# Optimization experiments

Measured on AMD Instinct MI355X. Metric: run time of the kernel, lower is better.

The kernel has to match this reference:

```python
import jax, jax.numpy as jnp
import numpy as np

DIM = 1024
SEQ_LEN = 4096
K = 256
HEADS = 16
DIM_HEAD = DIM // HEADS  # 64
BATCH = 4


def setup_inputs() -> dict:
    key = jax.random.key(0)
    ks = jax.random.split(key, 8)
    x = jax.random.normal(ks[0], (BATCH, SEQ_LEN, DIM), dtype=jnp.float32)
    # nn.Linear weights are [out, in]; y = x @ W.T
    std_lin = 1.0 / np.sqrt(DIM)
    Wq = jax.random.uniform(ks[1], (HEADS * DIM_HEAD, DIM), minval=-std_lin, maxval=std_lin, dtype=jnp.float32)
    Wk = jax.random.uniform(ks[2], (HEADS * DIM_HEAD, DIM), minval=-std_lin, maxval=std_lin, dtype=jnp.float32)
    Wv = jax.random.uniform(ks[3], (HEADS * DIM_HEAD, DIM), minval=-std_lin, maxval=std_lin, dtype=jnp.float32)
    # proj_k/proj_v init_: uniform(-1/sqrt(k), 1/sqrt(k)) on [seq_len, k]
    std_p = 1.0 / np.sqrt(K)
    proj_k = jax.random.uniform(ks[4], (SEQ_LEN, K), minval=-std_p, maxval=std_p, dtype=jnp.float32)
    proj_v = jax.random.uniform(ks[5], (SEQ_LEN, K), minval=-std_p, maxval=std_p, dtype=jnp.float32)
    std_o = 1.0 / np.sqrt(HEADS * DIM_HEAD)
    Wo = jax.random.uniform(ks[6], (DIM, HEADS * DIM_HEAD), minval=-std_o, maxval=std_o, dtype=jnp.float32)
    bo = jax.random.uniform(ks[7], (DIM,), minval=-std_o, maxval=std_o, dtype=jnp.float32)
    return {"x": x, "Wq": Wq, "Wk": Wk, "Wv": Wv, "proj_k": proj_k, "proj_v": proj_v, "Wo": Wo, "bo": bo}


def reference(x, Wq, Wk, Wv, proj_k, proj_v, Wo, bo):
    b, n, d = x.shape
    h, dh, k = HEADS, DIM_HEAD, K
    # q/k/v projections
    q = jnp.einsum('bnd,ed->bne', x, Wq)            # [b, n, h*dh]
    keys = jnp.einsum('bnd,ed->bne', x, Wk)         # [b, n, h*dh]
    vals = jnp.einsum('bnd,ed->bne', x, Wv)         # [b, n, h*dh]
    # low-rank projection along sequence: [b, n, e] x [n, k] -> [b, k, e]
    keys = jnp.einsum('bne,nk->bke', keys, proj_k[:n])
    vals = jnp.einsum('bne,nk->bke', vals, proj_v[:n])
    # split heads
    q = q.reshape(b, n, h, dh).transpose(0, 2, 1, 3)        # [b, h, n, dh]
    keys = keys.reshape(b, k, h, dh).transpose(0, 2, 1, 3)  # [b, h, k, dh]
    vals = vals.reshape(b, k, h, dh).transpose(0, 2, 1, 3)  # [b, h, k, dh]
    dots = jnp.einsum('bhnd,bhkd->bhnk', q, keys) * (dh ** -0.5)
    attn = jax.nn.softmax(dots, axis=-1)
    out = jnp.einsum('bhnk,bhkd->bhnd', attn, vals)
    out = out.transpose(0, 2, 1, 3).reshape(b, n, h * dh)
    return jnp.einsum('bne,oe->bno', out, Wo) + bo
```

## Files before the change

### kernel.cpp

```cpp
#include <hip/hip_runtime.h>
#include <hip/hip_bf16.h>
#include <stdint.h>

typedef unsigned short u16;
typedef __attribute__((ext_vector_type(8))) short bf16x8;
typedef __attribute__((ext_vector_type(4))) float f32x4;

#define DEV __device__ __forceinline__

DEV u16 f2bf(float f) {
  union { float f; unsigned u; } v; v.f = f;
  unsigned r = (v.u + 0x7fffu + ((v.u >> 16) & 1u)) >> 16;
  return (u16)r;
}

DEV float bf2f(u16 h) {
  union { unsigned u; float f; } v; v.u = ((unsigned)h) << 16;
  return v.f;
}

DEV unsigned pk2(float lo, float hi) {
  union { __hip_bfloat162 h; unsigned u; } c;
  c.h = __float22bfloat162_rn(make_float2(lo, hi));
  return c.u;
}

DEV f32x4 mfma16(bf16x8 a, bf16x8 b, f32x4 c) {
  return __builtin_amdgcn_mfma_f32_16x16x32_bf16(a, b, c, 0, 0, 0);
}

DEV void gload_lds16(const u16* g, u16* l) {
  __builtin_amdgcn_global_load_lds((const __attribute__((address_space(1))) void*)g,
                                   (__attribute__((address_space(3))) void*)l, 16, 0, 0);
}

#define QSCALE 0.18033688011112042f

__global__ void cvt_xpose_kernel(const float* __restrict__ src, u16* __restrict__ dst_rm,
                                 u16* __restrict__ dst_tp, int R, int C,
                                 long zS, long zRM, long zTP) {
  __shared__ u16 tile[64][72];
  src += (size_t)blockIdx.z * zS;
  dst_tp += (size_t)blockIdx.z * zTP;
  int r0 = blockIdx.y * 64, c0 = blockIdx.x * 64;
  int tr = threadIdx.x >> 2, tc = (threadIdx.x & 3) * 16;
  const float* s = src + (size_t)(r0 + tr) * C + c0 + tc;
  u16 loc[16];
#pragma unroll
  for (int q = 0; q < 4; ++q) {
    float4 v = ((const float4*)s)[q];
    loc[q * 4 + 0] = f2bf(v.x); loc[q * 4 + 1] = f2bf(v.y);
    loc[q * 4 + 2] = f2bf(v.z); loc[q * 4 + 3] = f2bf(v.w);
  }
#pragma unroll
  for (int i = 0; i < 16; ++i) tile[tr][tc + i] = loc[i];
  if (dst_rm) {
    u16* d = dst_rm + (size_t)blockIdx.z * zRM + (size_t)(r0 + tr) * C + c0 + tc;
    *(bf16x8*)d = *(const bf16x8*)&loc[0];
    *(bf16x8*)(d + 8) = *(const bf16x8*)&loc[8];
  }
  __syncthreads();
  u16 tmp[16];
#pragma unroll
  for (int i = 0; i < 16; ++i) tmp[i] = tile[tc + i][tr];
  u16* d = dst_tp + (size_t)(c0 + tr) * R + r0 + tc;
  *(bf16x8*)d = *(const bf16x8*)&tmp[0];
  *(bf16x8*)(d + 8) = *(const bf16x8*)&tmp[8];
}

__global__ void cvt_misc_kernel(const float* __restrict__ s0, const float* __restrict__ s1,
                                const float* __restrict__ s2, const float* __restrict__ s3,
                                u16* __restrict__ d0, u16* __restrict__ d1,
                                u16* __restrict__ d2, u16* __restrict__ d3,
                                const float* __restrict__ pk, const float* __restrict__ pv,
                                u16* __restrict__ projT) {
  __shared__ u16 tile[64][72];
  const int y = blockIdx.y;
  if (y < 4) {
    const float* s; u16* d;
    switch (y) {
      case 0: s = s0; d = d0; break;
      case 1: s = s1; d = d1; break;
      case 2: s = s2; d = d2; break;
      default: s = s3; d = d3; break;
    }
    int i = blockIdx.x * 256 + threadIdx.x;
    float4 v = ((const float4*)s)[i];
    ushort4 o; o.x = f2bf(v.x); o.y = f2bf(v.y); o.z = f2bf(v.z); o.w = f2bf(v.w);
    ((ushort4*)d)[i] = o;
    return;
  }
  if (blockIdx.x >= 256) return;
  const float* src = (y == 4) ? pk : pv;
  u16* dst = projT + (size_t)(y - 4) * 1048576;
  int r0 = (blockIdx.x >> 2) * 64, c0 = (blockIdx.x & 3) * 64;
  int tr = threadIdx.x >> 2, tc = (threadIdx.x & 3) * 16;
  const float* s = src + (size_t)(r0 + tr) * 256 + c0 + tc;
  u16 loc[16];
#pragma unroll
  for (int q = 0; q < 4; ++q) {
    float4 v = ((const float4*)s)[q];
    loc[q * 4 + 0] = f2bf(v.x); loc[q * 4 + 1] = f2bf(v.y);
    loc[q * 4 + 2] = f2bf(v.z); loc[q * 4 + 3] = f2bf(v.w);
  }
#pragma unroll
  for (int i = 0; i < 16; ++i) tile[tr][tc + i] = loc[i];
  __syncthreads();
  u16 tmp[16];
#pragma unroll
  for (int i = 0; i < 16; ++i) tmp[i] = tile[tc + i][tr];
  u16* d = dst + (size_t)(c0 + tr) * 4096 + r0 + tc;
  *(bf16x8*)d = *(const bf16x8*)&tmp[0];
  *(bf16x8*)(d + 8) = *(const bf16x8*)&tmp[8];
}

__global__ void reduce4_kernel(const u16* __restrict__ part, u16* __restrict__ out) {
  int i = blockIdx.x * 256 + threadIdx.x;
  bf16x8 a = ((const bf16x8*)part)[i];
  bf16x8 b = ((const bf16x8*)part)[i + 262144];
  bf16x8 c = ((const bf16x8*)part)[i + 524288];
  bf16x8 d = ((const bf16x8*)part)[i + 786432];
  u16 o[8];
#pragma unroll
  for (int j = 0; j < 8; ++j)
    o[j] = f2bf(bf2f((u16)a[j]) + bf2f((u16)b[j]) + bf2f((u16)c[j]) + bf2f((u16)d[j]));
  ((bf16x8*)out)[i] = *(const bf16x8*)&o[0];
}

template<int OMODE>
__global__ __launch_bounds__(256, 4)
void gemm_bt_kernel(const u16* __restrict__ A, const u16* __restrict__ Bt,
                    const u16* __restrict__ Bt2, void* __restrict__ Cout,
                    u16* __restrict__ CoutT, const float* __restrict__ bias, float cscale,
                    int ldA, int ldB, int ldC, int Klen,
                    long zA, long zB, long zC, int bMod, long kChunkA, long kChunkB) {
  __shared__ __align__(16) u16 smA[2][128 * 32];
  __shared__ __align__(16) u16 smB[2][128 * 32];
  const int t = threadIdx.x;
  const int lane = t & 63, wave = t >> 6;
  const int wm = wave & 1, wn = wave >> 1;
  const int g = lane >> 4, r = lane & 15;
  const int id = blockIdx.y * gridDim.x + blockIdx.x;
  const int cpx = (gridDim.x * gridDim.y) >> 3;
  const int s = (id & 7) * cpx + (id >> 3);
  const int bx = s % gridDim.x, by = s / gridDim.x;
  const int z = blockIdx.z;
  const int b = z % bMod, kc = z / bMod;
  const u16* Ab = A + (size_t)b * zA + (size_t)kc * kChunkA;
  const u16* Bbase = (Bt2 && (b & 1)) ? Bt2 : Bt;
  const u16* Bb = Bbase + (size_t)b * zB + (size_t)kc * kChunkB;
  const int m0 = by * 128, n0 = bx * 128;
  const int srow = t >> 2;
  const int lslot = ((t & 3) + 4 - ((srow >> 1) & 3)) & 3;

  f32x4 acc[4][4];
#pragma unroll
  for (int m = 0; m < 4; ++m)
#pragma unroll
    for (int n = 0; n < 4; ++n) acc[m][n] = f32x4{0.f, 0.f, 0.f, 0.f};

  auto STAGE = [&](int buf, int k0) {
#pragma unroll
    for (int p = 0; p < 2; ++p) {
      int row = p * 64 + srow;
      gload_lds16(Ab + (size_t)(m0 + row) * ldA + k0 + lslot * 8, &smA[buf][p * 2048 + wave * 512]);
      gload_lds16(Bb + (size_t)(n0 + row) * ldB + k0 + lslot * 8, &smB[buf][p * 2048 + wave * 512]);
    }
  };

  const int nt = Klen >> 5;
  STAGE(0, 0);
  __syncthreads();
  int cur = 0;
  for (int it = 0; it < nt; ++it) {
    if (it + 1 < nt) STAGE(cur ^ 1, (it + 1) << 5);
    bf16x8 af[4], bfr[4];
#pragma unroll
    for (int m = 0; m < 4; ++m) {
      int row = wm * 64 + m * 16 + r;
      int ps = (g + (row >> 1)) & 3;
      af[m] = *(const bf16x8*)&smA[cur][row * 32 + ps * 8];
    }
#pragma unroll
    for (int n = 0; n < 4; ++n) {
      int row = wn * 64 + n * 16 + r;
      int ps = (g + (row >> 1)) & 3;
      bfr[n] = *(const bf16x8*)&smB[cur][row * 32 + ps * 8];
    }
#pragma unroll
    for (int m = 0; m < 4; ++m)
#pragma unroll
      for (int n = 0; n < 4; ++n)
        acc[m][n] = mfma16(af[m], bfr[n], acc[m][n]);
    __syncthreads();
    cur ^= 1;
  }

  if constexpr (OMODE == 4) {
    u16* myT = (u16*)&smA[0][0] + wave * 4096;
    u16* Cg = (u16*)Cout + (size_t)z * zC + (size_t)(m0 + wm * 64) * ldC + n0 + wn * 64;
#pragma unroll
    for (int m = 0; m < 4; ++m)
#pragma unroll
      for (int n = 0; n < 4; ++n)
#pragma unroll
        for (int rr = 0; rr < 4; ++rr) {
          int rl = m * 16 + 4 * g + rr;
          int cl = n * 16 + r;
          myT[rl * 64 + (((cl >> 3) ^ (rl & 7)) << 3) + (cl & 7)] = f2bf(acc[m][n][rr]);
        }
#pragma unroll
    for (int i = 0; i < 8; ++i) {
      int idx = i * 64 + lane;
      int row = idx >> 3, c8 = idx & 7;
      bf16x8 v = *(const bf16x8*)&myT[row * 64 + ((c8 ^ (row & 7)) << 3)];
      *(bf16x8*)&Cg[(size_t)row * ldC + c8 * 8] = v;
    }
  } else {
    if ((z & 1) == 0) {
      u16* C = (u16*)Cout + (size_t)(z >> 1) * zC;
#pragma unroll
      for (int n = 0; n < 4; ++n) {
        int col = n0 + wn * 64 + n * 16 + r;
#pragma unroll
        for (int m = 0; m < 4; ++m) {
          int rowb = m0 + wm * 64 + m * 16 + 4 * g;
#pragma unroll
          for (int rr = 0; rr < 4; ++rr)
            C[(size_t)(rowb + rr) * ldC + col] = f2bf(acc[m][n][rr]);
        }
      }
    } else {
      u16* C = CoutT + (size_t)(z >> 1) * zC;
#pragma unroll
      for (int n = 0; n < 4; ++n) {
        int col = n0 + wn * 64 + n * 16 + r;
#pragma unroll
        for (int m = 0; m < 4; ++m) {
          int rowb = m0 + wm * 64 + m * 16 + 4 * g;
          ushort4 o;
          o.x = f2bf(acc[m][n][0]); o.y = f2bf(acc[m][n][1]);
          o.z = f2bf(acc[m][n][2]); o.w = f2bf(acc[m][n][3]);
          *(ushort4*)&C[(size_t)col * 256 + rowb] = o;
        }
      }
    }
  }
}

template<int OMODE>
__global__ __launch_bounds__(256, 2)
void qgemm64_kernel(const u16* __restrict__ A, const u16* __restrict__ Bt,
                    void* __restrict__ Cout, const float* __restrict__ bias,
                    float cscale, int ldA, int ldB, int ldC, int Klen) {
  __shared__ __align__(16) u16 lds[32768];
  const int t = threadIdx.x;
  const int lane = t & 63, wave = t >> 6;
  const int g = lane >> 4, r = lane & 15;
  const int wm = wave >> 1, wn = wave & 1;
  const int id = blockIdx.y * gridDim.x + blockIdx.x;
  const int cpx = (gridDim.x * gridDim.y) >> 3;
  const int s = (id & 7) * cpx + (id >> 3);
  const int bx = s & 7, by = s >> 3;
  const int m0 = by * 128, n0 = bx * 128;

  auto STAGE = [&](int buf, int k0) {
#pragma unroll
    for (int j = 0; j < 4; ++j) {
      int u = j * 256 + t;
      int row = u >> 3, psl = u & 7;
      int sl = (psl + 8 - (row & 7)) & 7;
      gload_lds16(A + (size_t)(m0 + row) * ldA + k0 + sl * 8,
                  lds + buf * 16384 + u * 8);
    }
#pragma unroll
    for (int j = 0; j < 4; ++j) {
      int u = j * 256 + t;
      int row = u >> 3, psl = u & 7;
      int sl = (psl + 8 - (row & 7)) & 7;
      gload_lds16(Bt + (size_t)(n0 + row) * ldB + k0 + sl * 8,
                  lds + buf * 16384 + 8192 + u * 8);
    }
  };

  f32x4 acc[4][4];
#pragma unroll
  for (int m = 0; m < 4; ++m)
#pragma unroll
    for (int n = 0; n < 4; ++n) acc[m][n] = f32x4{0.f, 0.f, 0.f, 0.f};

  const int nt = Klen >> 6;
  STAGE(0, 0);
  asm volatile("s_waitcnt vmcnt(0)" ::: "memory");
  __builtin_amdgcn_s_barrier();

  int cur = 0;
  for (int it = 0; it < nt; ++it) {
    if (it + 1 < nt) STAGE(cur ^ 1, (it + 1) << 6);
    const u16* Ab = lds + cur * 16384;
    const u16* Bb = Ab + 8192;
    bf16x8 af[4][2], bfr[4][2];
#pragma unroll
    for (int m = 0; m < 4; ++m) {
      int row = wm * 64 + m * 16 + r;
      af[m][0] = *(const bf16x8*)&Ab[row * 64 + (((g + row) & 7) << 3)];
      af[m][1] = *(const bf16x8*)&Ab[row * 64 + (((4 + g + row) & 7) << 3)];
    }
#pragma unroll
    for (int n = 0; n < 4; ++n) {
      int row = wn * 64 + n * 16 + r;
      bfr[n][0] = *(const bf16x8*)&Bb[row * 64 + (((g + row) & 7) << 3)];
      bfr[n][1] = *(const bf16x8*)&Bb[row * 64 + (((4 + g + row) & 7) << 3)];
    }
#pragma unroll
    for (int m = 0; m < 4; ++m)
#pragma unroll
      for (int n = 0; n < 4; ++n) {
        acc[m][n] = mfma16(af[m][0], bfr[n][0], acc[m][n]);
        acc[m][n] = mfma16(af[m][1], bfr[n][1], acc[m][n]);
      }
    if (it + 1 < nt) {
      asm volatile("s_waitcnt vmcnt(0)" ::: "memory");
      __builtin_amdgcn_s_barrier();
    }
    cur ^= 1;
  }
  __builtin_amdgcn_s_barrier();

  if constexpr (OMODE == 0) {
    u16* myT = lds + wave * 4096;
    u16* Cg = (u16*)Cout + (size_t)(m0 + wm * 64) * ldC + n0 + wn * 64;
#pragma unroll
    for (int m = 0; m < 4; ++m)
#pragma unroll
      for (int n = 0; n < 4; ++n)
#pragma unroll
        for (int rr = 0; rr < 4; ++rr) {
          int rl = m * 16 + 4 * g + rr;
          int cl = n * 16 + r;
          myT[rl * 64 + (((cl >> 3) ^ (rl & 7)) << 3) + (cl & 7)] = f2bf(acc[m][n][rr] * cscale);
        }
#pragma unroll
    for (int i = 0; i < 8; ++i) {
      int idx = i * 64 + lane;
      int row = idx >> 3, c8 = idx & 7;
      bf16x8 v = *(const bf16x8*)&myT[row * 64 + ((c8 ^ (row & 7)) << 3)];
      *(bf16x8*)&Cg[(size_t)row * ldC + c8 * 8] = v;
    }
  } else {
    float* myF = (float*)lds + wave * 2048;
    float bvn[4];
#pragma unroll
    for (int n = 0; n < 4; ++n) bvn[n] = bias[n0 + wn * 64 + n * 16 + r];
    float* Cg = (float*)Cout + (size_t)(m0 + wm * 64) * ldC + n0 + wn * 64;
#pragma unroll
    for (int np = 0; np < 2; ++np) {
#pragma unroll
      for (int n2 = 0; n2 < 2; ++n2)
#pragma unroll
        for (int m = 0; m < 4; ++m)
#pragma unroll
          for (int rr = 0; rr < 4; ++rr) {
            int rl = m * 16 + 4 * g + rr;
            int cl = n2 * 16 + r;
            myF[rl * 32 + ((((cl >> 2) ^ (rl & 7)) & 7) << 2) + (cl & 3)] =
                acc[m][np * 2 + n2][rr] + bvn[np * 2 + n2];
          }
#pragma unroll
      for (int i = 0; i < 8; ++i) {
        int idx = i * 64 + lane;
        int row = idx >> 3, c = idx & 7;
        float4 v = *(const float4*)&myF[row * 32 + (((c ^ (row & 7)) & 7) << 2)];
        *(float4*)&Cg[(size_t)row * ldC + np * 32 + c * 4] = v;
      }
    }
  }
}

__global__ __launch_bounds__(256, 3)
void attn_kernel(const u16* __restrict__ Q, const u16* __restrict__ Kl,
                 const u16* __restrict__ VT, u16* __restrict__ Out) {
  __shared__ __align__(16) u16 sm[24576];
  const int t = threadIdx.x, lane = t & 63, w = t >> 6;
  const int g = lane >> 4, r = lane & 15;
  const int id = (blockIdx.y << 6) | blockIdx.x;
  const int s = (id & 7) * (gridDim.y << 3) + (id >> 3);
  const int b = blockIdx.z, h = s >> 6, n0 = (s & 63) * 64;
  const u16* Kb = Kl + (size_t)b * 262144 + h * 64;
  const u16* Vb = VT + (size_t)b * 262144 + (size_t)(h * 64) * 256;
  u16* vbase = sm + 16384;

  auto stage_slice = [&](int sl64, int buf) {
#pragma unroll
    for (int i = 0; i < 2; ++i) {
      int u = i * 256 + t;
      int d = u >> 3, ps = u & 7;
      gload_lds16(Vb + (size_t)d * 256 + sl64 * 64 + (ps ^ (d & 7)) * 8,
                  vbase + buf * 4096 + i * 2048 + t * 8);
    }
  };

#pragma unroll
  for (int p = 0; p < 8; ++p) {
    int row = p * 32 + (t >> 3);
    int ls = ((t & 7) + 8 - (row & 7)) & 7;
    gload_lds16(Kb + (size_t)row * 1024 + ls * 8, sm + p * 2048 + w * 512);
  }
  stage_slice(0, 0);
  stage_slice(1, 1);
  const int qrow = n0 + w * 16 + r;
  const u16* Qp = Q + ((size_t)(b * 4096 + qrow)) * 1024 + h * 64 + g * 8;
  bf16x8 aq0 = *(const bf16x8*)Qp;
  bf16x8 aq1 = *(const bf16x8*)(Qp + 32);
  asm volatile("s_waitcnt vmcnt(4)" ::: "memory");
  __builtin_amdgcn_s_barrier();

  f32x4 dotv[16];
  __builtin_amdgcn_s_setprio(1);
#pragma unroll
  for (int kf = 0; kf < 16; ++kf) {
    int row = kf * 16 + r;
    bf16x8 kb0 = *(const bf16x8*)&sm[row * 64 + ((g + row) & 7) * 8];
    bf16x8 kb1 = *(const bf16x8*)&sm[row * 64 + ((4 + g + row) & 7) * 8];
    f32x4 d = f32x4{0.f, 0.f, 0.f, 0.f};
    d = mfma16(kb0, aq0, d);
    d = mfma16(kb1, aq1, d);
    dotv[kf] = d;
  }
  __builtin_amdgcn_s_setprio(0);
  asm volatile("s_waitcnt vmcnt(2)" ::: "memory");
  __builtin_amdgcn_s_barrier();

  float mx = -3.4e38f;
#pragma unroll
  for (int kf = 0; kf < 16; ++kf)
    mx = fmaxf(mx, fmaxf(fmaxf(dotv[kf][0], dotv[kf][1]), fmaxf(dotv[kf][2], dotv[kf][3])));
  mx = fmaxf(mx, __shfl_xor(mx, 16, 64));
  mx = fmaxf(mx, __shfl_xor(mx, 32, 64));
  float ssum = 0.f;
#pragma unroll
  for (int kf = 0; kf < 16; ++kf)
#pragma unroll
    for (int j = 0; j < 4; ++j) {
      float p = __builtin_amdgcn_exp2f(dotv[kf][j] - mx);
      dotv[kf][j] = p;
      ssum += p;
    }
  ssum += __shfl_xor(ssum, 16, 64);
  ssum += __shfl_xor(ssum, 32, 64);
  const float inv = 1.f / ssum;
  float invv[4];
#pragma unroll
  for (int rr = 0; rr < 4; ++rr) invv[rr] = __shfl(inv, 4 * g + rr, 64);

  const int q16 = w * 16 + r;
  const int qx = (q16 & 7) << 3;
#pragma unroll
  for (int kf = 0; kf < 16; ++kf) {
    uint2 val;
    val.x = pk2(dotv[kf][0], dotv[kf][1]);
    val.y = pk2(dotv[kf][2], dotv[kf][3]);
    *(uint2*)&sm[(q16 * 256 + kf * 16 + 4 * g) ^ qx] = val;
  }

  f32x4 oacc[4];
#pragma unroll
  for (int df = 0; df < 4; ++df) oacc[df] = f32x4{0.f, 0.f, 0.f, 0.f};
#pragma unroll
  for (int ph = 0; ph < 4; ++ph) {
    const u16* vb = vbase + (ph & 1) * 4096;
    __builtin_amdgcn_s_setprio(1);
#pragma unroll
    for (int kk2 = 0; kk2 < 2; ++kk2) {
      int kk = ph * 2 + kk2;
      bf16x8 ap = *(const bf16x8*)&sm[(q16 * 256 + kk * 32 + g * 8) ^ qx];
#pragma unroll
      for (int df = 0; df < 4; ++df) {
        int d = df * 16 + r;
        bf16x8 bv = *(const bf16x8*)&vb[d * 64 + ((kk2 * 4 + g) ^ (d & 7)) * 8];
        oacc[df] = mfma16(ap, bv, oacc[df]);
      }
    }
    __builtin_amdgcn_s_setprio(0);
    if (ph < 3) {
      asm volatile("s_waitcnt vmcnt(0)" ::: "memory");
      __builtin_amdgcn_s_barrier();
      if (ph < 2) stage_slice(ph + 2, ph & 1);
    }
  }

  u16* myO = sm + w * 4096;
#pragma unroll
  for (int df = 0; df < 4; ++df)
#pragma unroll
    for (int rr = 0; rr < 4; ++rr) {
      int row = 4 * g + rr;
      int col = df * 16 + r;
      myO[row * 64 + (((col >> 3) ^ (row & 7)) << 3) + (col & 7)] = f2bf(oacc[df][rr] * invv[rr]);
    }
#pragma unroll
  for (int i = 0; i < 2; ++i) {
    int idx = i * 64 + lane;
    int row = idx >> 3, c8 = idx & 7;
    bf16x8 v = *(const bf16x8*)&myO[row * 64 + ((c8 ^ (row & 7)) << 3)];
    *(bf16x8*)&Out[((size_t)(b * 4096 + n0 + w * 16 + row)) * 1024 + h * 64 + c8 * 8] = v;
  }
}

extern "C" void kernel_launch(void* const* d_in, const int* in_sizes, int n_in,
                              void* d_out, int out_size, void* d_ws, size_t ws_size,
                              hipStream_t stream) {
  const float* x  = (const float*)d_in[0];
  const float* Wq = (const float*)d_in[1];
  const float* Wk = (const float*)d_in[2];
  const float* Wv = (const float*)d_in[3];
  const float* pk = (const float*)d_in[4];
  const float* pv = (const float*)d_in[5];
  const float* Wo = (const float*)d_in[6];
  const float* bo = (const float*)d_in[7];

  u16* ws = (u16*)d_ws;
  u16* xbf   = ws;
  u16* xT    = xbf + 16777216;
  u16* wqb   = xT + 16777216;
  u16* wkb   = wqb + 1048576;
  u16* wvb   = wkb + 1048576;
  u16* wob   = wvb + 1048576;
  u16* projT = wob + 1048576;
  u16* Qb    = projT + 2097152;
  u16* xp    = Qb + 16777216;
  u16* klow  = xp + 2097152;
  u16* vT    = klow + 1048576;
  u16* aout  = xbf;
  u16* xp_part = Qb;

  cvt_xpose_kernel<<<dim3(16, 64, 4), 256, 0, stream>>>(x, xbf, xT, 4096, 1024,
                                                        4194304, 4194304, 4194304);
  cvt_misc_kernel<<<dim3(1024, 6), 256, 0, stream>>>(Wq, Wk, Wv, Wo, wqb, wkb, wvb, wob,
                                                     pk, pv, projT);
  gemm_bt_kernel<4><<<dim3(32, 4, 4), 256, 0, stream>>>(
      projT, xT, nullptr, (void*)xp_part, nullptr, nullptr, 1.f,
      4096, 4096, 4096, 1024, 0, 0, 2097152, 1, 1024, 1024);
  reduce4_kernel<<<1024, 256, 0, stream>>>(xp_part, xp);
  gemm_bt_kernel<3><<<dim3(8, 2, 8), 256, 0, stream>>>(
      xp, wkb, wvb, (void*)klow, vT, nullptr, 1.f,
      4096, 1024, 1024, 1024, 1048576, 0, 262144, 2, 1024, 0);
  qgemm64_kernel<0><<<dim3(8, 128), 256, 0, stream>>>(
      xbf, wqb, (void*)Qb, nullptr, QSCALE, 1024, 1024, 1024, 1024);
  attn_kernel<<<dim3(64, 16, 4), 256, 0, stream>>>(Qb, klow, vT, aout);
  qgemm64_kernel<1><<<dim3(8, 128), 256, 0, stream>>>(
      aout, wob, d_out, bo, 1.f, 1024, 1024, 1024, 1024);
}
```

Measured before the change: 201.7 us.

## Fuse K/V low-rank GEMM and Q projection GEMM into one launch

Merges the small K/V low-rank projection GEMM (128 blocks) and the Q projection GEMM (1024 blocks) into a single kernel launch, with blocks dispatched by blockIdx.y. This removes one launch and lets the small, under-filled K/V GEMM overlap with the Q GEMM instead of running alone on a mostly idle GPU. The trade-off is that the fused kernel runs at the occupancy of the larger-LDS path (launch bounds 2) for both halves, and the templates are specialized away.

```diff
diff --git a/kernel.cpp b/kernel.cpp
--- a/kernel.cpp
+++ b/kernel.cpp
@@ -127,13 +127,10 @@
   ((bf16x8*)out)[i] = *(const bf16x8*)&o[0];
 }
 
-template<int OMODE>
 __global__ __launch_bounds__(256, 4)
 void gemm_bt_kernel(const u16* __restrict__ A, const u16* __restrict__ Bt,
-                    const u16* __restrict__ Bt2, void* __restrict__ Cout,
-                    u16* __restrict__ CoutT, const float* __restrict__ bias, float cscale,
-                    int ldA, int ldB, int ldC, int Klen,
-                    long zA, long zB, long zC, int bMod, long kChunkA, long kChunkB) {
+                    void* __restrict__ Cout, int ldA, int ldB, int ldC, int Klen,
+                    long zC, long kChunkA, long kChunkB) {
   __shared__ __align__(16) u16 smA[2][128 * 32];
   __shared__ __align__(16) u16 smB[2][128 * 32];
   const int t = threadIdx.x;
@@ -145,10 +142,8 @@
   const int s = (id & 7) * cpx + (id >> 3);
   const int bx = s % gridDim.x, by = s / gridDim.x;
   const int z = blockIdx.z;
-  const int b = z % bMod, kc = z / bMod;
-  const u16* Ab = A + (size_t)b * zA + (size_t)kc * kChunkA;
-  const u16* Bbase = (Bt2 && (b & 1)) ? Bt2 : Bt;
-  const u16* Bb = Bbase + (size_t)b * zB + (size_t)kc * kChunkB;
+  const u16* Ab = A + (size_t)z * kChunkA;
+  const u16* Bb = Bt + (size_t)z * kChunkB;
   const int m0 = by * 128, n0 = bx * 128;
   const int srow = t >> 2;
   const int lslot = ((t & 3) + 4 - ((srow >> 1) & 3)) & 3;
@@ -196,29 +191,99 @@
     cur ^= 1;
   }
 
-  if constexpr (OMODE == 4) {
-    u16* myT = (u16*)&smA[0][0] + wave * 4096;
-    u16* Cg = (u16*)Cout + (size_t)z * zC + (size_t)(m0 + wm * 64) * ldC + n0 + wn * 64;
+  u16* myT = (u16*)&smA[0][0] + wave * 4096;
+  u16* Cg = (u16*)Cout + (size_t)z * zC + (size_t)(m0 + wm * 64) * ldC + n0 + wn * 64;
+#pragma unroll
+  for (int m = 0; m < 4; ++m)
+#pragma unroll
+    for (int n = 0; n < 4; ++n)
+#pragma unroll
+      for (int rr = 0; rr < 4; ++rr) {
+        int rl = m * 16 + 4 * g + rr;
+        int cl = n * 16 + r;
+        myT[rl * 64 + (((cl >> 3) ^ (rl & 7)) << 3) + (cl & 7)] = f2bf(acc[m][n][rr]);
+      }
+#pragma unroll
+  for (int i = 0; i < 8; ++i) {
+    int idx = i * 64 + lane;
+    int row = idx >> 3, c8 = idx & 7;
+    bf16x8 v = *(const bf16x8*)&myT[row * 64 + ((c8 ^ (row & 7)) << 3)];
+    *(bf16x8*)&Cg[(size_t)row * ldC + c8 * 8] = v;
+  }
+}
+
+__global__ __launch_bounds__(256, 2)
+void qkv_fused_kernel(const u16* __restrict__ A, const u16* __restrict__ Wq,
+                      u16* __restrict__ Qout, float cscale,
+                      const u16* __restrict__ xp, const u16* __restrict__ wk,
+                      const u16* __restrict__ wv, u16* __restrict__ klow,
+                      u16* __restrict__ vT) {
+  __shared__ __align__(16) u16 lds[32768];
+  const int t = threadIdx.x;
+  const int lane = t & 63, wave = t >> 6;
+  const int g = lane >> 4, r = lane & 15;
+
+  if (blockIdx.y < 16) {
+    const int idx = blockIdx.y * 8 + blockIdx.x;
+    const int z = idx >> 4, id2 = idx & 15;
+    const int s2 = (id2 & 7) * 2 + (id2 >> 3);
+    const int bx2 = s2 & 7, by2 = s2 >> 3;
+    const int bb = z & 1, kc = z >> 1;
+    const u16* Ab = xp + (size_t)bb * 1048576 + (size_t)kc * 1024;
+    const u16* Bb = bb ? wv : wk;
+    const int m0 = by2 * 128, n0 = bx2 * 128;
+    const int wm = wave & 1, wn = wave >> 1;
+    const int srow = t >> 2;
+    const int lslot = ((t & 3) + 4 - ((srow >> 1) & 3)) & 3;
+
+    f32x4 acc[4][4];
 #pragma unroll
     for (int m = 0; m < 4; ++m)
 #pragma unroll
-      for (int n = 0; n < 4; ++n)
-#pragma unroll
-        for (int rr = 0; rr < 4; ++rr) {
-          int rl = m * 16 + 4 * g + rr;
-          int cl = n * 16 + r;
-          myT[rl * 64 + (((cl >> 3) ^ (rl & 7)) << 3) + (cl & 7)] = f2bf(acc[m][n][rr]);
-        }
-#pragma unroll
-    for (int i = 0; i < 8; ++i) {
-      int idx = i * 64 + lane;
-      int row = idx >> 3, c8 = idx & 7;
-      bf16x8 v = *(const bf16x8*)&myT[row * 64 + ((c8 ^ (row & 7)) << 3)];
-      *(bf16x8*)&Cg[(size_t)row * ldC + c8 * 8] = v;
-    }
-  } else {
-    if ((z & 1) == 0) {
-      u16* C = (u16*)Cout + (size_t)(z >> 1) * zC;
+      for (int n = 0; n < 4; ++n) acc[m][n] = f32x4{0.f, 0.f, 0.f, 0.f};
+
+    auto STAGE = [&](int buf, int k0) {
+#pragma unroll
+      for (int p = 0; p < 2; ++p) {
+        int row = p * 64 + srow;
+        gload_lds16(Ab + (size_t)(m0 + row) * 4096 + k0 + lslot * 8,
+                    lds + buf * 4096 + p * 2048 + wave * 512);
+        gload_lds16(Bb + (size_t)(n0 + row) * 1024 + k0 + lslot * 8,
+                    lds + 8192 + buf * 4096 + p * 2048 + wave * 512);
+      }
+    };
+
+    STAGE(0, 0);
+    __syncthreads();
+    int cur = 0;
+    for (int it = 0; it < 32; ++it) {
+      if (it + 1 < 32) STAGE(cur ^ 1, (it + 1) << 5);
+      const u16* sA = lds + cur * 4096;
+      const u16* sB = lds + 8192 + cur * 4096;
+      bf16x8 af[4], bfr[4];
+#pragma unroll
+      for (int m = 0; m < 4; ++m) {
+        int row = wm * 64 + m * 16 + r;
+        int ps = (g + (row >> 1)) & 3;
+        af[m] = *(const bf16x8*)&sA[row * 32 + ps * 8];
+      }
+#pragma unroll
+      for (int n = 0; n < 4; ++n) {
+        int row = wn * 64 + n * 16 + r;
+        int ps = (g + (row >> 1)) & 3;
+        bfr[n] = *(const bf16x8*)&sB[row * 32 + ps * 8];
+      }
+#pragma unroll
+      for (int m = 0; m < 4; ++m)
+#pragma unroll
+        for (int n = 0; n < 4; ++n)
+          acc[m][n] = mfma16(af[m], bfr[n], acc[m][n]);
+      __syncthreads();
+      cur ^= 1;
+    }
+
+    if (bb == 0) {
+      u16* C = klow + (size_t)kc * 262144;
 #pragma unroll
       for (int n = 0; n < 4; ++n) {
         int col = n0 + wn * 64 + n * 16 + r;
@@ -227,11 +292,11 @@
           int rowb = m0 + wm * 64 + m * 16 + 4 * g;
 #pragma unroll
           for (int rr = 0; rr < 4; ++rr)
-            C[(size_t)(rowb + rr) * ldC + col] = f2bf(acc[m][n][rr]);
+            C[(size_t)(rowb + rr) * 1024 + col] = f2bf(acc[m][n][rr]);
         }
       }
     } else {
-      u16* C = CoutT + (size_t)(z >> 1) * zC;
+      u16* C = vT + (size_t)kc * 262144;
 #pragma unroll
       for (int n = 0; n < 4; ++n) {
         int col = n0 + wn * 64 + n * 16 + r;
@@ -245,14 +310,102 @@
         }
       }
     }
-  }
-}
-
-template<int OMODE>
+    return;
+  }
+
+  const int wm = wave >> 1, wn = wave & 1;
+  const int id = (blockIdx.y - 16) * 8 + blockIdx.x;
+  const int s = (id & 7) * 128 + (id >> 3);
+  const int bx = s & 7, by = s >> 3;
+  const int m0 = by * 128, n0 = bx * 128;
+
+  auto STAGE = [&](int buf, int k0) {
+#pragma unroll
+    for (int j = 0; j < 4; ++j) {
+      int u = j * 256 + t;
+      int row = u >> 3, psl = u & 7;
+      int sl = (psl + 8 - (row & 7)) & 7;
+      gload_lds16(A + (size_t)(m0 + row) * 1024 + k0 + sl * 8,
+                  lds + buf * 16384 + u * 8);
+    }
+#pragma unroll
+    for (int j = 0; j < 4; ++j) {
+      int u = j * 256 + t;
+      int row = u >> 3, psl = u & 7;
+      int sl = (psl + 8 - (row & 7)) & 7;
+      gload_lds16(Wq + (size_t)(n0 + row) * 1024 + k0 + sl * 8,
+                  lds + buf * 16384 + 8192 + u * 8);
+    }
+  };
+
+  f32x4 acc[4][4];
+#pragma unroll
+  for (int m = 0; m < 4; ++m)
+#pragma unroll
+    for (int n = 0; n < 4; ++n) acc[m][n] = f32x4{0.f, 0.f, 0.f, 0.f};
+
+  STAGE(0, 0);
+  asm volatile("s_waitcnt vmcnt(0)" ::: "memory");
+  __builtin_amdgcn_s_barrier();
+
+  int cur = 0;
+  for (int it = 0; it < 16; ++it) {
+    if (it + 1 < 16) STAGE(cur ^ 1, (it + 1) << 6);
+    const u16* Ab = lds + cur * 16384;
+    const u16* Bb = Ab + 8192;
+    bf16x8 af[4][2], bfr[4][2];
+#pragma unroll
+    for (int m = 0; m < 4; ++m) {
+      int row = wm * 64 + m * 16 + r;
+      af[m][0] = *(const bf16x8*)&Ab[row * 64 + (((g + row) & 7) << 3)];
+      af[m][1] = *(const bf16x8*)&Ab[row * 64 + (((4 + g + row) & 7) << 3)];
+    }
+#pragma unroll
+    for (int n = 0; n < 4; ++n) {
+      int row = wn * 64 + n * 16 + r;
+      bfr[n][0] = *(const bf16x8*)&Bb[row * 64 + (((g + row) & 7) << 3)];
+      bfr[n][1] = *(const bf16x8*)&Bb[row * 64 + (((4 + g + row) & 7) << 3)];
+    }
+#pragma unroll
+    for (int m = 0; m < 4; ++m)
+#pragma unroll
+      for (int n = 0; n < 4; ++n) {
+        acc[m][n] = mfma16(af[m][0], bfr[n][0], acc[m][n]);
+        acc[m][n] = mfma16(af[m][1], bfr[n][1], acc[m][n]);
+      }
+    if (it + 1 < 16) {
+      asm volatile("s_waitcnt vmcnt(0)" ::: "memory");
+      __builtin_amdgcn_s_barrier();
+    }
+    cur ^= 1;
+  }
+  __builtin_amdgcn_s_barrier();
+
+  u16* myT = lds + wave * 4096;
+  u16* Cg = Qout + (size_t)(m0 + wm * 64) * 1024 + n0 + wn * 64;
+#pragma unroll
+  for (int m = 0; m < 4; ++m)
+#pragma unroll
+    for (int n = 0; n < 4; ++n)
+#pragma unroll
+      for (int rr = 0; rr < 4; ++rr) {
+        int rl = m * 16 + 4 * g + rr;
+        int cl = n * 16 + r;
+        myT[rl * 64 + (((cl >> 3) ^ (rl & 7)) << 3) + (cl & 7)] = f2bf(acc[m][n][rr] * cscale);
+      }
+#pragma unroll
+  for (int i = 0; i < 8; ++i) {
+    int idx = i * 64 + lane;
+    int row = idx >> 3, c8 = idx & 7;
+    bf16x8 v = *(const bf16x8*)&myT[row * 64 + ((c8 ^ (row & 7)) << 3)];
+    *(bf16x8*)&Cg[(size_t)row * 1024 + c8 * 8] = v;
+  }
+}
+
 __global__ __launch_bounds__(256, 2)
 void qgemm64_kernel(const u16* __restrict__ A, const u16* __restrict__ Bt,
-                    void* __restrict__ Cout, const float* __restrict__ bias,
-                    float cscale, int ldA, int ldB, int ldC, int Klen) {
+                    float* __restrict__ Cout, const float* __restrict__ bias,
+                    int ldA, int ldB, int ldC, int Klen) {
   __shared__ __align__(16) u16 lds[32768];
   const int t = threadIdx.x;
   const int lane = t & 63, wave = t >> 6;
@@ -327,52 +480,30 @@
   }
   __builtin_amdgcn_s_barrier();
 
-  if constexpr (OMODE == 0) {
-    u16* myT = lds + wave * 4096;
-    u16* Cg = (u16*)Cout + (size_t)(m0 + wm * 64) * ldC + n0 + wn * 64;
-#pragma unroll
-    for (int m = 0; m < 4; ++m)
-#pragma unroll
-      for (int n = 0; n < 4; ++n)
+  float* myF = (float*)lds + wave * 2048;
+  float bvn[4];
+#pragma unroll
+  for (int n = 0; n < 4; ++n) bvn[n] = bias[n0 + wn * 64 + n * 16 + r];
+  float* Cg = Cout + (size_t)(m0 + wm * 64) * ldC + n0 + wn * 64;
+#pragma unroll
+  for (int np = 0; np < 2; ++np) {
+#pragma unroll
+    for (int n2 = 0; n2 < 2; ++n2)
+#pragma unroll
+      for (int m = 0; m < 4; ++m)
 #pragma unroll
         for (int rr = 0; rr < 4; ++rr) {
           int rl = m * 16 + 4 * g + rr;
-          int cl = n * 16 + r;
-          myT[rl * 64 + (((cl >> 3) ^ (rl & 7)) << 3) + (cl & 7)] = f2bf(acc[m][n][rr] * cscale);
+          int cl = n2 * 16 + r;
+          myF[rl * 32 + ((((cl >> 2) ^ (rl & 7)) & 7) << 2) + (cl & 3)] =
+              acc[m][np * 2 + n2][rr] + bvn[np * 2 + n2];
         }
 #pragma unroll
     for (int i = 0; i < 8; ++i) {
       int idx = i * 64 + lane;
-      int row = idx >> 3, c8 = idx & 7;
-      bf16x8 v = *(const bf16x8*)&myT[row * 64 + ((c8 ^ (row & 7)) << 3)];
-      *(bf16x8*)&Cg[(size_t)row * ldC + c8 * 8] = v;
-    }
-  } else {
-    float* myF = (float*)lds + wave * 2048;
-    float bvn[4];
-#pragma unroll
-    for (int n = 0; n < 4; ++n) bvn[n] = bias[n0 + wn * 64 + n * 16 + r];
-    float* Cg = (float*)Cout + (size_t)(m0 + wm * 64) * ldC + n0 + wn * 64;
-#pragma unroll
-    for (int np = 0; np < 2; ++np) {
-#pragma unroll
-      for (int n2 = 0; n2 < 2; ++n2)
-#pragma unroll
-        for (int m = 0; m < 4; ++m)
-#pragma unroll
-          for (int rr = 0; rr < 4; ++rr) {
-            int rl = m * 16 + 4 * g + rr;
-            int cl = n2 * 16 + r;
-            myF[rl * 32 + ((((cl >> 2) ^ (rl & 7)) & 7) << 2) + (cl & 3)] =
-                acc[m][np * 2 + n2][rr] + bvn[np * 2 + n2];
-          }
-#pragma unroll
-      for (int i = 0; i < 8; ++i) {
-        int idx = i * 64 + lane;
-        int row = idx >> 3, c = idx & 7;
-        float4 v = *(const float4*)&myF[row * 32 + (((c ^ (row & 7)) & 7) << 2)];
-        *(float4*)&Cg[(size_t)row * ldC + np * 32 + c * 4] = v;
-      }
+      int row = idx >> 3, c = idx & 7;
+      float4 v = *(const float4*)&myF[row * 32 + (((c ^ (row & 7)) & 7) << 2)];
+      *(float4*)&Cg[(size_t)row * ldC + np * 32 + c * 4] = v;
     }
   }
 }
@@ -538,16 +669,12 @@
                                                         4194304, 4194304, 4194304);
   cvt_misc_kernel<<<dim3(1024, 6), 256, 0, stream>>>(Wq, Wk, Wv, Wo, wqb, wkb, wvb, wob,
                                                      pk, pv, projT);
-  gemm_bt_kernel<4><<<dim3(32, 4, 4), 256, 0, stream>>>(
-      projT, xT, nullptr, (void*)xp_part, nullptr, nullptr, 1.f,
-      4096, 4096, 4096, 1024, 0, 0, 2097152, 1, 1024, 1024);
+  gemm_bt_kernel<<<dim3(32, 4, 4), 256, 0, stream>>>(
+      projT, xT, (void*)xp_part, 4096, 4096, 4096, 1024, 2097152, 1024, 1024);
   reduce4_kernel<<<1024, 256, 0, stream>>>(xp_part, xp);
-  gemm_bt_kernel<3><<<dim3(8, 2, 8), 256, 0, stream>>>(
-      xp, wkb, wvb, (void*)klow, vT, nullptr, 1.f,
-      4096, 1024, 1024, 1024, 1048576, 0, 262144, 2, 1024, 0);
-  qgemm64_kernel<0><<<dim3(8, 128), 256, 0, stream>>>(
-      xbf, wqb, (void*)Qb, nullptr, QSCALE, 1024, 1024, 1024, 1024);
+  qkv_fused_kernel<<<dim3(8, 144), 256, 0, stream>>>(
+      xbf, wqb, Qb, QSCALE, xp, wkb, wvb, klow, vT);
   attn_kernel<<<dim3(64, 16, 4), 256, 0, stream>>>(Qb, klow, vT, aout);
-  qgemm64_kernel<1><<<dim3(8, 128), 256, 0, stream>>>(
-      aout, wob, d_out, bo, 1.f, 1024, 1024, 1024, 1024);
-}
+  qgemm64_kernel<<<dim3(8, 128), 256, 0, stream>>>(
+      aout, wob, (float*)d_out, bo, 1024, 1024, 1024, 1024);
+}
```

Result: no change. 200.1 us (-0.8%).
